# Optimization experiments

Measured on AMD Instinct MI355X. Metric: run time of the kernel, lower is better.

Reference implementation:

```python
import jax, jax.numpy as jnp
import numpy as np


def setup_inputs() -> dict:
    key = jax.random.key(0)
    k1, k2, k3 = jax.random.split(key, 3)
    in_features, out_features = 256, 256
    x = jax.random.normal(k1, (16, 128, in_features), dtype=jnp.float32)
    # weight[:, :, 0] = output mixing weights, weight[:, :, 1] = frequency weights
    weight = jax.random.normal(k2, (in_features, out_features, 2), dtype=jnp.float32) / np.sqrt(in_features)
    # bias[0] = output bias, bias[1:] = per-(in,out) phase
    bias = jax.random.normal(k3, (in_features + 1, out_features), dtype=jnp.float32) / np.sqrt(in_features)
    return {"x": x, "weight": weight, "bias": bias}


def reference(x, weight, bias):
    out_features = weight.shape[1]
    out_shape = x.shape[:-1] + (out_features,)
    xf = x.reshape(-1, x.shape[-1])  # [B, I]
    w_amp = weight[:, :, 0]   # [I, O]
    w_freq = weight[:, :, 1]  # [I, O]
    # bio = sin(x_bi * w_io + phase_io); out_bo = sum_i amp_io * bio
    bio = jnp.sin(jnp.einsum('bi,io->bio', xf, w_freq) + bias[1:, :])
    out = jnp.einsum('io,bio->bo', w_amp, bio) + bias[0, :]
    return out.reshape(out_shape)
```

## Files before the change

### kernel.cpp

```cpp
#include <hip/hip_runtime.h>


constexpr int IN_F   = 256;
constexpr int OUT_F  = 256;
constexpr int BROWS  = 2048;
constexpr int BTILE  = 8;
constexpr int ISPLIT = 8;
constexpr int ICHUNK = IN_F / ISPLIT;
constexpr int OPAIRS = 64;

#define INV2PI 0.15915494309189535f

__global__ __launch_bounds__(OPAIRS * ISPLIT, 4) void ripple_kernel(
    const float* __restrict__ x,
    const float* __restrict__ weight,
    const float* __restrict__ bias,
    float* __restrict__ out)
{
    const int tx = threadIdx.x;
    const int g  = threadIdx.y;
    const int ob = blockIdx.x & 1;
    const int bb = blockIdx.x >> 1;
    const int b0 = bb * BTILE;
    const int oc = ob * OPAIRS + tx;

    __shared__ __align__(16) float xs_t[BTILE * IN_F];
    __shared__ float2 red[4][BTILE][OPAIRS];

    {
        const int t  = g * OPAIRS + tx;
        const int r  = t >> 6;
        const int c4 = t & 63;
        const float4 v = ((const float4*)x)[(b0 + r) * (IN_F / 4) + c4];
        xs_t[(4 * c4 + 0) * BTILE + r] = v.x * INV2PI;
        xs_t[(4 * c4 + 1) * BTILE + r] = v.y * INV2PI;
        xs_t[(4 * c4 + 2) * BTILE + r] = v.z * INV2PI;
        xs_t[(4 * c4 + 3) * BTILE + r] = v.w * INV2PI;
    }
    __syncthreads();

    float acc0[BTILE], acc1[BTILE];
#pragma unroll
    for (int r = 0; r < BTILE; ++r) { acc0[r] = 0.0f; acc1[r] = 0.0f; }

    const float4* __restrict__ wq  = (const float4*)weight;
    const float2* __restrict__ ph2 = (const float2*)bias;

    const int i0 = g * ICHUNK;
#pragma unroll 4
    for (int ii = 0; ii < ICHUNK; ++ii) {
        const int i = i0 + ii;
        const float4 w = wq[i * (OUT_F / 2) + oc];
        const float2 p = ph2[(i + 1) * (OUT_F / 2) + oc];
        const float px = p.x * INV2PI;
        const float py = p.y * INV2PI;
        const float4 xa = *(const float4*)&xs_t[i * BTILE];
        const float4 xb = *(const float4*)&xs_t[i * BTILE + 4];
        const float xv[BTILE] = {xa.x, xa.y, xa.z, xa.w, xb.x, xb.y, xb.z, xb.w};
#pragma unroll
        for (int r = 0; r < BTILE; ++r) {
            acc0[r] += w.x * __builtin_amdgcn_sinf(fmaf(xv[r], w.y, px));
            acc1[r] += w.z * __builtin_amdgcn_sinf(fmaf(xv[r], w.w, py));
        }
    }

    if (g >= 4) {
#pragma unroll
        for (int r = 0; r < BTILE; ++r) red[g - 4][r][tx] = make_float2(acc0[r], acc1[r]);
    }
    __syncthreads();
    if (g < 4) {
#pragma unroll
        for (int r = 0; r < BTILE; ++r) { float2 t = red[g][r][tx]; acc0[r] += t.x; acc1[r] += t.y; }
    }
    __syncthreads();
    if (g == 2 || g == 3) {
#pragma unroll
        for (int r = 0; r < BTILE; ++r) red[g - 2][r][tx] = make_float2(acc0[r], acc1[r]);
    }
    __syncthreads();
    if (g < 2) {
#pragma unroll
        for (int r = 0; r < BTILE; ++r) { float2 t = red[g][r][tx]; acc0[r] += t.x; acc1[r] += t.y; }
    }
    __syncthreads();
    if (g == 1) {
#pragma unroll
        for (int r = 0; r < BTILE; ++r) red[0][r][tx] = make_float2(acc0[r], acc1[r]);
    }
    __syncthreads();
    if (g == 0) {
        const float2 bo = ph2[oc];
#pragma unroll
        for (int r = 0; r < BTILE; ++r) {
            float2 t = red[0][r][tx];
            float2 v = make_float2(acc0[r] + t.x + bo.x, acc1[r] + t.y + bo.y);
            ((float2*)out)[(b0 + r) * (OUT_F / 2) + oc] = v;
        }
    }
}

extern "C" void kernel_launch(void* const* d_in, const int* in_sizes, int n_in,
                              void* d_out, int out_size, void* d_ws, size_t ws_size,
                              hipStream_t stream) {
    const float* x      = (const float*)d_in[0];
    const float* weight = (const float*)d_in[1];
    const float* bias   = (const float*)d_in[2];
    float* out          = (float*)d_out;

    dim3 grid((BROWS / BTILE) * 2);
    dim3 block(OPAIRS, ISPLIT);
    ripple_kernel<<<grid, block, 0, stream>>>(x, weight, bias, out);
}
```

Measured before the change: 75.26 us.

## Split outputs four ways, deepen input split, reduce partials via wave shuffles

The output dimension is now split across four blocks instead of two, with 32 output pairs per block, and the input dimension across 16 thread groups instead of 8. This doubles the grid and raises occupancy hints. The multi-stage shared-memory tree reduction is replaced by a cross-half-wave shuffle followed by a single shared-memory round and a serial sum in the first group, which removes several barriers. The x staging is remapped to fit the new thread shape. In exchange, the shared x tile is loaded redundantly by more blocks and the final per-thread serial reduction is longer.

Result: slower. 76.97 us (+2.3%).

```diff
diff --git a/kernel.cpp b/kernel.cpp
--- a/kernel.cpp
+++ b/kernel.cpp
@@ -5,13 +5,14 @@
 constexpr int OUT_F  = 256;
 constexpr int BROWS  = 2048;
 constexpr int BTILE  = 8;
-constexpr int ISPLIT = 8;
+constexpr int ISPLIT = 16;
 constexpr int ICHUNK = IN_F / ISPLIT;
-constexpr int OPAIRS = 64;
+constexpr int OPAIRS = 32;
+constexpr int OSPLIT = 4;
 
 #define INV2PI 0.15915494309189535f
 
-__global__ __launch_bounds__(OPAIRS * ISPLIT, 4) void ripple_kernel(
+__global__ __launch_bounds__(OPAIRS * ISPLIT, 8) void ripple_kernel(
     const float* __restrict__ x,
     const float* __restrict__ weight,
     const float* __restrict__ bias,
@@ -19,23 +20,23 @@
 {
     const int tx = threadIdx.x;
     const int g  = threadIdx.y;
-    const int ob = blockIdx.x & 1;
-    const int bb = blockIdx.x >> 1;
+    const int ob = blockIdx.x & (OSPLIT - 1);
+    const int bb = blockIdx.x >> 2;
     const int b0 = bb * BTILE;
     const int oc = ob * OPAIRS + tx;
 
-    __shared__ __align__(16) float xs_t[BTILE * IN_F];
-    __shared__ float2 red[4][BTILE][OPAIRS];
+    __shared__ __align__(16) float xs_t[IN_F * BTILE];
+    __shared__ float2 red[ISPLIT / 2 - 1][BTILE][OPAIRS];
 
     {
         const int t  = g * OPAIRS + tx;
-        const int r  = t >> 6;
-        const int c4 = t & 63;
-        const float4 v = ((const float4*)x)[(b0 + r) * (IN_F / 4) + c4];
-        xs_t[(4 * c4 + 0) * BTILE + r] = v.x * INV2PI;
-        xs_t[(4 * c4 + 1) * BTILE + r] = v.y * INV2PI;
-        xs_t[(4 * c4 + 2) * BTILE + r] = v.z * INV2PI;
-        xs_t[(4 * c4 + 3) * BTILE + r] = v.w * INV2PI;
+        const int r  = t & 7;
+        const int i4 = t >> 3;
+        const float4 v = ((const float4*)x)[(b0 + r) * (IN_F / 4) + i4];
+        xs_t[(4 * i4 + 0) * BTILE + r] = v.x * INV2PI;
+        xs_t[(4 * i4 + 1) * BTILE + r] = v.y * INV2PI;
+        xs_t[(4 * i4 + 2) * BTILE + r] = v.z * INV2PI;
+        xs_t[(4 * i4 + 3) * BTILE + r] = v.w * INV2PI;
     }
     __syncthreads();
 
@@ -47,7 +48,7 @@
     const float2* __restrict__ ph2 = (const float2*)bias;
 
     const int i0 = g * ICHUNK;
-#pragma unroll 4
+#pragma unroll 2
     for (int ii = 0; ii < ICHUNK; ++ii) {
         const int i = i0 + ii;
         const float4 w = wq[i * (OUT_F / 2) + oc];
@@ -64,38 +65,29 @@
         }
     }
 
-    if (g >= 4) {
 #pragma unroll
-        for (int r = 0; r < BTILE; ++r) red[g - 4][r][tx] = make_float2(acc0[r], acc1[r]);
+    for (int r = 0; r < BTILE; ++r) {
+        acc0[r] += __shfl_down(acc0[r], 32);
+        acc1[r] += __shfl_down(acc1[r], 32);
     }
-    __syncthreads();
-    if (g < 4) {
+
+    const int wv = g >> 1;
+    if ((g & 1) == 0 && wv > 0) {
 #pragma unroll
-        for (int r = 0; r < BTILE; ++r) { float2 t = red[g][r][tx]; acc0[r] += t.x; acc1[r] += t.y; }
-    }
-    __syncthreads();
-    if (g == 2 || g == 3) {
-#pragma unroll
-        for (int r = 0; r < BTILE; ++r) red[g - 2][r][tx] = make_float2(acc0[r], acc1[r]);
-    }
-    __syncthreads();
-    if (g < 2) {
-#pragma unroll
-        for (int r = 0; r < BTILE; ++r) { float2 t = red[g][r][tx]; acc0[r] += t.x; acc1[r] += t.y; }
-    }
-    __syncthreads();
-    if (g == 1) {
-#pragma unroll
-        for (int r = 0; r < BTILE; ++r) red[0][r][tx] = make_float2(acc0[r], acc1[r]);
+        for (int r = 0; r < BTILE; ++r) red[wv - 1][r][tx] = make_float2(acc0[r], acc1[r]);
     }
     __syncthreads();
     if (g == 0) {
         const float2 bo = ph2[oc];
 #pragma unroll
         for (int r = 0; r < BTILE; ++r) {
-            float2 t = red[0][r][tx];
-            float2 v = make_float2(acc0[r] + t.x + bo.x, acc1[r] + t.y + bo.y);
-            ((float2*)out)[(b0 + r) * (OUT_F / 2) + oc] = v;
+            float s0 = acc0[r], s1 = acc1[r];
+#pragma unroll
+            for (int k = 0; k < ISPLIT / 2 - 1; ++k) {
+                const float2 t = red[k][r][tx];
+                s0 += t.x; s1 += t.y;
+            }
+            ((float2*)out)[(b0 + r) * (OUT_F / 2) + oc] = make_float2(s0 + bo.x, s1 + bo.y);
         }
     }
 }
@@ -108,7 +100,7 @@
     const float* bias   = (const float*)d_in[2];
     float* out          = (float*)d_out;
 
-    dim3 grid((BROWS / BTILE) * 2);
+    dim3 grid((BROWS / BTILE) * OSPLIT);
     dim3 block(OPAIRS, ISPLIT);
     ripple_kernel<<<grid, block, 0, stream>>>(x, weight, bias, out);
 }
```
